# Performance work log

Hardware: AMD Instinct MI355X
Metric: run time of the kernel (lower is better)

The kernel has to match this reference:

```python
import jax, jax.numpy as jnp
import numpy as np

B, W, H = 8, 1024, 1024
NUM_LABELS = 100  # mask ids in [0, NUM_LABELS); 0 = background
EPS = 1e-7


def setup_inputs() -> dict:
    key = jax.random.key(0)
    k1, k2 = jax.random.split(key)
    pred = jax.random.normal(k1, (B, 2, W, H), dtype=jnp.float32)
    mask = jax.random.randint(k2, (B, W, H), 0, NUM_LABELS, dtype=jnp.int32)
    ignored_map = jnp.ones((B, W, H), dtype=jnp.float32)
    return {"pred": pred, "mask": mask, "ignored_map": ignored_map}


def _smooth_l1(d):
    # SmoothL1Loss(reduction='none'), beta=1
    a = jnp.abs(d)
    return jnp.where(a < 1.0, 0.5 * d * d, a - 0.5)


def _gt_single(mask2d):
    # Vectorized replacement of the per-instance python loop:
    # segment-mean for centroids, segment-max for the per-instance `norm`.
    seg = mask2d.reshape(-1)  # [W*H]
    x_map = jnp.tile(jnp.arange(H, dtype=jnp.float32), W)    # column index (x)
    y_map = jnp.repeat(jnp.arange(W, dtype=jnp.float32), H)  # row index (y)
    cnt = jax.ops.segment_sum(jnp.ones_like(x_map), seg, num_segments=NUM_LABELS)
    safe_cnt = jnp.maximum(cnt, 1.0)
    xc = (jax.ops.segment_sum(x_map, seg, num_segments=NUM_LABELS) / safe_cnt)[seg]
    yc = (jax.ops.segment_sum(y_map, seg, num_segments=NUM_LABELS) / safe_cnt)[seg]
    fg = (seg != 0).astype(jnp.float32)  # label 0 is background (index_list[1:])
    vx = (x_map - xc) * fg  # (x_map - mean_x) * nuclei, instances are disjoint
    vy = (y_map - yc) * fg
    # torch.max over the whole image of (coord - c)*nuclei == max(seg_max, 0)
    mx = jnp.maximum(jax.ops.segment_max(vx, seg, num_segments=NUM_LABELS), 0.0)
    my = jnp.maximum(jax.ops.segment_max(vy, seg, num_segments=NUM_LABELS), 0.0)
    gx = vx / jnp.where(mx == 0.0, 1.0, mx)[seg]  # norm(): divide by max iff max != 0
    gy = vy / jnp.where(my == 0.0, 1.0, my)[seg]
    return jnp.stack([gx, gy]).reshape(2, W, H)


def reference(pred, mask, ignored_map):
    gt = jax.vmap(_gt_single)(mask)  # [B, 2, W, H]
    fg = (mask != 0).astype(jnp.float32)[:, None]  # [B, 1, W, H]
    bg = 1.0 - fg
    n = float(mask.size)
    # ((mask != 0) + 1e-07).sum() == fg_count + eps * numel
    fg_den = jnp.sum(fg) + EPS * n
    bg_den = jnp.sum(bg) + EPS * n
    d = _smooth_l1(pred - gt)
    ig = ignored_map[:, None]
    offset_loss = jnp.sum(d * ig * (fg / fg_den + bg / bg_den))
    return offset_loss, gt
```

## Files before the change

kernel.cpp:

```cpp
#include <hip/hip_runtime.h>

#define NL 100
#define BB 8
#define HH 1024
#define NPIX (1024 * 1024)
#define EPSF 1e-7f
#define NBLK 128
#define LGX 256
#define NLOSS (LGX * BB)

typedef float f4 __attribute__((ext_vector_type(4)));

#define OFF_ACC  0
#define OFF_TKT  1
#define OFF_TAB  16
#define OFF_CNT0 (OFF_TAB + 4 * BB * NL)
#define OFF_M8   (OFF_CNT0 + BB + 8)
#define OFF_PART (OFF_M8 + BB * (NPIX / 4))

__device__ __forceinline__ int part_idx(int v, int blk, int b, int l) {
    return ((v * NBLK + blk) * BB + b) * NL + l;
}

__global__ __launch_bounds__(256) void k_stats(const int* __restrict__ mask,
                                               unsigned* __restrict__ wsu) {
    __shared__ unsigned s_cs[4][2][NL];
    __shared__ unsigned s_mx[4][NL];
    __shared__ unsigned g_cnt[NL], g_sx[NL], g_sy[NL], g_mx[NL], g_my[NL];
    unsigned* part = wsu + OFF_PART;
    unsigned* m8   = wsu + OFF_M8;
    const int b    = blockIdx.y;
    const int blk  = blockIdx.x;
    const int wv   = threadIdx.x >> 6;
    const int lane = threadIdx.x & 63;
    if (blk == 0 && b == 0 && threadIdx.x == 0) {
        wsu[OFF_ACC] = 0u;
        wsu[OFF_TKT] = 0u;
    }
    for (int i = threadIdx.x; i < NL; i += 256) {
        g_cnt[i] = 0u; g_sx[i] = 0u; g_sy[i] = 0u; g_mx[i] = 0u; g_my[i] = 0u;
    }
    for (int i = lane; i < 2 * NL; i += 64) s_cs[wv][0][i] = 0u;
    for (int i = lane; i < NL; i += 64) s_mx[wv][i] = 0u;
    __syncthreads();

    const int4* m4  = (const int4*)(mask + (size_t)b * NPIX);
    unsigned*   m8b = m8 + (size_t)b * (NPIX / 4);
    const int y0 = blk * 8 + wv * 2;

    int4 R[2][4];
#pragma unroll
    for (int r = 0; r < 2; ++r)
#pragma unroll
        for (int it = 0; it < 4; ++it)
            R[r][it] = m4[(y0 + r) * 256 + it * 64 + lane];

#pragma unroll
    for (int r = 0; r < 2; ++r) {
        unsigned* tp = &s_cs[wv][r][0];
        unsigned* mp = &s_mx[wv][0];
        const int y = y0 + r;
#pragma unroll
        for (int it = 0; it < 4; ++it) {
            const int4 mv = R[r][it];
            const int c4 = it * 64 + lane;
            const unsigned v0 = (1u << 21) + (unsigned)(c4 << 2);
            atomicAdd(tp + mv.x, v0);      atomicMax(mp + mv.x, v0);
            atomicAdd(tp + mv.y, v0 + 1u); atomicMax(mp + mv.y, v0 + 1u);
            atomicAdd(tp + mv.z, v0 + 2u); atomicMax(mp + mv.z, v0 + 2u);
            atomicAdd(tp + mv.w, v0 + 3u); atomicMax(mp + mv.w, v0 + 3u);
            m8b[y * 256 + c4] = (unsigned)mv.x | ((unsigned)mv.y << 8) |
                                ((unsigned)mv.z << 16) | ((unsigned)mv.w << 24);
        }
    }
    for (int e = lane; e < NL; e += 64) {
        const unsigned cs0 = s_cs[wv][0][e];
        const unsigned cs1 = s_cs[wv][1][e];
        const unsigned c0 = cs0 >> 21, c1 = cs1 >> 21;
        const unsigned cnt = c0 + c1;
        if (cnt) {
            atomicAdd(&g_cnt[e], cnt);
            atomicAdd(&g_sx[e], (cs0 & 0x1FFFFFu) + (cs1 & 0x1FFFFFu));
            atomicAdd(&g_sy[e], c0 * (unsigned)y0 + c1 * (unsigned)(y0 + 1));
            atomicMax(&g_my[e], c1 ? (unsigned)(y0 + 1) : (unsigned)y0);
            atomicMax(&g_mx[e], s_mx[wv][e] & 0x1FFFFFu);
        }
    }
    __syncthreads();
    for (int e = threadIdx.x; e < NL; e += 256) {
        part[part_idx(0, blk, b, e)] = g_cnt[e];
        part[part_idx(1, blk, b, e)] = g_sx[e];
        part[part_idx(2, blk, b, e)] = g_sy[e];
        part[part_idx(3, blk, b, e)] = g_mx[e];
        part[part_idx(4, blk, b, e)] = g_my[e];
    }
}

__global__ __launch_bounds__(512) void k_final(unsigned* __restrict__ wsu) {
    __shared__ unsigned s_st[5][NL];
    const unsigned* part = wsu + OFF_PART;
    const int b = blockIdx.x;
    const int t = threadIdx.x;
    if (t < 5 * NL) {
        const int v = t / NL;
        const int l = t - v * NL;
        unsigned s = 0u, m = 0u;
#pragma unroll 4
        for (int k = 0; k < NBLK; ++k) {
            const unsigned u = part[part_idx(v, k, b, l)];
            s += u; m = max(m, u);
        }
        s_st[v][l] = (v >= 3) ? m : s;
    }
    __syncthreads();
    if (t < NL) {
        const unsigned cnt = s_st[0][t];
        const float sc = (float)(cnt ? cnt : 1u);
        const float xc = (float)s_st[1][t] / sc;
        const float yc = (float)s_st[2][t] / sc;
        float fmx = (float)s_st[3][t] - xc; if (fmx < 0.0f) fmx = 0.0f;
        float fmy = (float)s_st[4][t] - yc; if (fmy < 0.0f) fmy = 0.0f;
        f4 e;
        e.x = xc;
        e.y = yc;
        e.z = (fmx == 0.0f) ? 1.0f : 1.0f / fmx;
        e.w = (fmy == 0.0f) ? 1.0f : 1.0f / fmy;
        ((f4*)(wsu + OFF_TAB))[b * NL + t] = e;
        if (t == 0) wsu[OFF_CNT0 + b] = cnt;
    }
}

__global__ __launch_bounds__(256, 4) void k_loss(const float* __restrict__ pred,
                                                 const float* __restrict__ ig,
                                                 unsigned* __restrict__ wsu,
                                                 float* __restrict__ out) {
    __shared__ f4 s_tab[NL];
    __shared__ unsigned s_c0[BB];
    __shared__ float s_part[4];
    const unsigned* m8 = wsu + OFF_M8;
    const int b = blockIdx.y;
    const int tid = threadIdx.x;
    for (int i = tid; i < NL; i += 256)
        s_tab[i] = ((const f4*)(wsu + OFF_TAB))[b * NL + i];
    if (tid < BB) s_c0[tid] = wsu[OFF_CNT0 + tid];
    __syncthreads();
    float bgc = 0.0f;
#pragma unroll
    for (int i = 0; i < BB; ++i) bgc += (float)s_c0[i];
    const float n = (float)BB * (float)NPIX;
    const float inv_bg = 1.0f / (bgc + EPSF * n);
    const float inv_fg = 1.0f / ((n - bgc) + EPSF * n);

    const unsigned* m8b = m8 + (size_t)b * (NPIX / 4);
    const f4* ig4 = (const f4*)(ig + (size_t)b * NPIX);
    const f4* px4 = (const f4*)(pred + (size_t)(2 * b) * NPIX);
    const f4* py4 = (const f4*)(pred + (size_t)(2 * b + 1) * NPIX);
    f4* gx4 = (f4*)(out + 1 + (size_t)(2 * b) * NPIX);
    f4* gy4 = (f4*)(out + 1 + (size_t)(2 * b + 1) * NPIX);

    const int base = blockIdx.x * 1024;
    unsigned M8[4]; f4 IV[4], PX[4], PY[4];
#pragma unroll
    for (int it = 0; it < 4; ++it) {
        const int i4 = base + it * 256 + tid;
        M8[it] = m8b[i4];
        IV[it] = __builtin_nontemporal_load(&ig4[i4]);
        PX[it] = __builtin_nontemporal_load(&px4[i4]);
        PY[it] = __builtin_nontemporal_load(&py4[i4]);
    }

    float acc = 0.0f;
#pragma unroll
    for (int it = 0; it < 4; ++it) {
        const int i4 = base + it * 256 + tid;
        const int p  = i4 << 2;
        const float x0 = (float)(p & (HH - 1));
        const float y  = (float)(p >> 10);
        const float* igs = (const float*)&IV[it];
        const float* pxs = (const float*)&PX[it];
        const float* pys = (const float*)&PY[it];
        f4 gxv, gyv;
        float* gxa = (float*)&gxv;
        float* gya = (float*)&gyv;
#pragma unroll
        for (int j = 0; j < 4; ++j) {
            const int m = (int)((M8[it] >> (8 * j)) & 255u);
            const f4 t = s_tab[m];
            const float fgf = (m != 0) ? 1.0f : 0.0f;
            const float gx = (x0 + (float)j - t.x) * t.z * fgf;
            const float gy = (y - t.y) * t.w * fgf;
            const float w  = ((m != 0) ? inv_fg : inv_bg) * igs[j];
            const float dx = pxs[j] - gx;
            const float dy = pys[j] - gy;
            const float ax = fabsf(dx), ay = fabsf(dy);
            acc += ((ax < 1.0f) ? 0.5f * dx * dx : ax - 0.5f) * w
                 + ((ay < 1.0f) ? 0.5f * dy * dy : ay - 0.5f) * w;
            gxa[j] = gx;
            gya[j] = gy;
        }
        __builtin_nontemporal_store(gxv, &gx4[i4]);
        __builtin_nontemporal_store(gyv, &gy4[i4]);
    }
#pragma unroll
    for (int off = 32; off > 0; off >>= 1) acc += __shfl_down(acc, off, 64);
    const int lane = tid & 63, wv = tid >> 6;
    if (lane == 0) s_part[wv] = acc;
    __syncthreads();
    if (tid == 0) {
        const float s = s_part[0] + s_part[1] + s_part[2] + s_part[3];
        const float old = atomicAdd((float*)wsu + OFF_ACC, s);
        asm volatile("" : : "v"(old) : "memory");
        const unsigned t = atomicAdd(wsu + OFF_TKT, 1u);
        if (t == NLOSS - 1) {
            out[0] = atomicAdd((float*)wsu + OFF_ACC, 0.0f);
        }
    }
}

extern "C" void kernel_launch(void* const* d_in, const int* in_sizes, int n_in,
                              void* d_out, int out_size, void* d_ws, size_t ws_size,
                              hipStream_t stream) {
    const float* pred = (const float*)d_in[0];
    const int*   mask = (const int*)d_in[1];
    const float* ig   = (const float*)d_in[2];
    float* out = (float*)d_out;
    unsigned* wsu = (unsigned*)d_ws;

    k_stats<<<dim3(NBLK, BB), 256, 0, stream>>>(mask, wsu);
    k_final<<<BB, 512, 0, stream>>>(wsu);
    k_loss<<<dim3(LGX, BB), 256, 0, stream>>>(pred, ig, wsu, out);
}
```

Measured before the change: 209.9 us.

## Fold stats finalization into k_stats via last-block ticket; hierarchical loss reduction

Removes the separate k_final launch. Each stats block now atomically merges its per-label partials into a global table, and the last block per batch (found with a ticket counter) computes the centroid/norm table. The loss kernel's single global ticket and accumulator become per-batch counters on separate cache lines plus a second-level ticket, which spreads atomic contention. A hipMemsetAsync replaces the in-kernel zeroing. The cost is global atomics in every stats block and an extra memset node in place of a kernel launch.

Result: faster. 177.4 us (-15.5%).

```diff
diff --git a/kernel.cpp b/kernel.cpp
--- a/kernel.cpp
+++ b/kernel.cpp
@@ -7,19 +7,22 @@
 #define EPSF 1e-7f
 #define NBLK 128
 #define LGX 256
-#define NLOSS (LGX * BB)
 
 typedef float f4 __attribute__((ext_vector_type(4)));
 
-#define OFF_ACC  0
-#define OFF_TKT  1
-#define OFF_TAB  16
-#define OFF_CNT0 (OFF_TAB + 4 * BB * NL)
-#define OFF_M8   (OFF_CNT0 + BB + 8)
-#define OFF_PART (OFF_M8 + BB * (NPIX / 4))
-
-__device__ __forceinline__ int part_idx(int v, int blk, int b, int l) {
-    return ((v * NBLK + blk) * BB + b) * NL + l;
+#define OFF_GACC 0
+#define OFF_GTKT 1
+#define OFF_BACC 64
+#define OFF_BTKT 320
+#define OFF_STKT 576
+#define OFF_GST  1024
+#define OFF_TAB  5120
+#define OFF_CNT0 8320
+#define OFF_M8   8336
+#define ZERO_BYTES 20480
+
+__device__ __forceinline__ int gst_idx(int v, int b, int l) {
+    return (v * BB + b) * NL + l;
 }
 
 __global__ __launch_bounds__(256) void k_stats(const int* __restrict__ mask,
@@ -27,16 +30,14 @@
     __shared__ unsigned s_cs[4][2][NL];
     __shared__ unsigned s_mx[4][NL];
     __shared__ unsigned g_cnt[NL], g_sx[NL], g_sy[NL], g_mx[NL], g_my[NL];
-    unsigned* part = wsu + OFF_PART;
-    unsigned* m8   = wsu + OFF_M8;
+    __shared__ unsigned s_fin[5][NL];
+    __shared__ int s_last;
+    unsigned* gst = wsu + OFF_GST;
+    unsigned* m8  = wsu + OFF_M8;
     const int b    = blockIdx.y;
     const int blk  = blockIdx.x;
     const int wv   = threadIdx.x >> 6;
     const int lane = threadIdx.x & 63;
-    if (blk == 0 && b == 0 && threadIdx.x == 0) {
-        wsu[OFF_ACC] = 0u;
-        wsu[OFF_TKT] = 0u;
-    }
     for (int i = threadIdx.x; i < NL; i += 256) {
         g_cnt[i] = 0u; g_sx[i] = 0u; g_sy[i] = 0u; g_mx[i] = 0u; g_my[i] = 0u;
     }
@@ -87,46 +88,45 @@
         }
     }
     __syncthreads();
-    for (int e = threadIdx.x; e < NL; e += 256) {
-        part[part_idx(0, blk, b, e)] = g_cnt[e];
-        part[part_idx(1, blk, b, e)] = g_sx[e];
-        part[part_idx(2, blk, b, e)] = g_sy[e];
-        part[part_idx(3, blk, b, e)] = g_mx[e];
-        part[part_idx(4, blk, b, e)] = g_my[e];
-    }
-}
-
-__global__ __launch_bounds__(512) void k_final(unsigned* __restrict__ wsu) {
-    __shared__ unsigned s_st[5][NL];
-    const unsigned* part = wsu + OFF_PART;
-    const int b = blockIdx.x;
-    const int t = threadIdx.x;
-    if (t < 5 * NL) {
+    unsigned dummy = 0u;
+    for (int t = threadIdx.x; t < 5 * NL; t += 256) {
         const int v = t / NL;
         const int l = t - v * NL;
-        unsigned s = 0u, m = 0u;
-#pragma unroll 4
-        for (int k = 0; k < NBLK; ++k) {
-            const unsigned u = part[part_idx(v, k, b, l)];
-            s += u; m = max(m, u);
-        }
-        s_st[v][l] = (v >= 3) ? m : s;
-    }
-    __syncthreads();
-    if (t < NL) {
-        const unsigned cnt = s_st[0][t];
+        const unsigned u = (v == 0) ? g_cnt[l] : (v == 1) ? g_sx[l]
+                         : (v == 2) ? g_sy[l] : (v == 3) ? g_mx[l] : g_my[l];
+        if (u) {
+            dummy += (v < 3) ? atomicAdd(&gst[gst_idx(v, b, l)], u)
+                             : atomicMax(&gst[gst_idx(v, b, l)], u);
+        }
+    }
+    asm volatile("" : : "v"(dummy));
+    if (threadIdx.x == 0) {
+        const unsigned old = atomicAdd(wsu + OFF_STKT + b * 32, 1u);
+        s_last = (old == NBLK - 1) ? 1 : 0;
+    }
+    __syncthreads();
+    if (!s_last) return;
+    for (int t = threadIdx.x; t < 5 * NL; t += 256) {
+        const int v = t / NL;
+        const int l = t - v * NL;
+        s_fin[v][l] = atomicAdd(&gst[gst_idx(v, b, l)], 0u);
+    }
+    __syncthreads();
+    if (threadIdx.x < NL) {
+        const int l = threadIdx.x;
+        const unsigned cnt = s_fin[0][l];
         const float sc = (float)(cnt ? cnt : 1u);
-        const float xc = (float)s_st[1][t] / sc;
-        const float yc = (float)s_st[2][t] / sc;
-        float fmx = (float)s_st[3][t] - xc; if (fmx < 0.0f) fmx = 0.0f;
-        float fmy = (float)s_st[4][t] - yc; if (fmy < 0.0f) fmy = 0.0f;
+        const float xc = (float)s_fin[1][l] / sc;
+        const float yc = (float)s_fin[2][l] / sc;
+        float fmx = (float)s_fin[3][l] - xc; if (fmx < 0.0f) fmx = 0.0f;
+        float fmy = (float)s_fin[4][l] - yc; if (fmy < 0.0f) fmy = 0.0f;
         f4 e;
         e.x = xc;
         e.y = yc;
         e.z = (fmx == 0.0f) ? 1.0f : 1.0f / fmx;
         e.w = (fmy == 0.0f) ? 1.0f : 1.0f / fmy;
-        ((f4*)(wsu + OFF_TAB))[b * NL + t] = e;
-        if (t == 0) wsu[OFF_CNT0 + b] = cnt;
+        ((f4*)(wsu + OFF_TAB))[b * NL + l] = e;
+        if (l == 0) wsu[OFF_CNT0 + b] = cnt;
     }
 }
 
@@ -208,11 +208,17 @@
     __syncthreads();
     if (tid == 0) {
         const float s = s_part[0] + s_part[1] + s_part[2] + s_part[3];
-        const float old = atomicAdd((float*)wsu + OFF_ACC, s);
-        asm volatile("" : : "v"(old) : "memory");
-        const unsigned t = atomicAdd(wsu + OFF_TKT, 1u);
-        if (t == NLOSS - 1) {
-            out[0] = atomicAdd((float*)wsu + OFF_ACC, 0.0f);
+        float* bacc = (float*)wsu + OFF_BACC + b * 32;
+        const float old = atomicAdd(bacc, s);
+        asm volatile("" : : "v"(old));
+        const unsigned t = atomicAdd(wsu + OFF_BTKT + b * 32, 1u);
+        if (t == LGX - 1) {
+            const float tb = atomicAdd(bacc, 0.0f);
+            const float o2 = atomicAdd((float*)wsu + OFF_GACC, tb);
+            asm volatile("" : : "v"(o2));
+            const unsigned t2 = atomicAdd(wsu + OFF_GTKT, 1u);
+            if (t2 == BB - 1)
+                out[0] = atomicAdd((float*)wsu + OFF_GACC, 0.0f);
         }
     }
 }
@@ -226,7 +232,7 @@
     float* out = (float*)d_out;
     unsigned* wsu = (unsigned*)d_ws;
 
+    (void)hipMemsetAsync(d_ws, 0, ZERO_BYTES, stream);
     k_stats<<<dim3(NBLK, BB), 256, 0, stream>>>(mask, wsu);
-    k_final<<<BB, 512, 0, stream>>>(wsu);
     k_loss<<<dim3(LGX, BB), 256, 0, stream>>>(pred, ig, wsu, out);
 }
```
